# Performance work log

Hardware: AMD Instinct MI355X
Metric: run time of the kernel (lower is better)

The kernel has to match this reference:

```python
import jax, jax.numpy as jnp
import numpy as np

HIDDEN = 2048
N_HEADS = 32
N_KV = 8
HEAD_DIM = HIDDEN // N_HEADS  # 64
GROUP = N_HEADS // N_KV       # 4
FFN = 8192
EPS = 1e-5
ROPE_BASE = 500000.0
NEG = -1e9


def rms_norm(x, w, eps=EPS):
    var = jnp.mean(x * x, axis=-1, keepdims=True)
    return x * jax.lax.rsqrt(var + eps) * w


def rope_cos_sin(position_ids):
    # inv_freq: [head_dim//2]
    inv_freq = 1.0 / (ROPE_BASE ** (jnp.arange(0, HEAD_DIM, 2, dtype=jnp.float32) / HEAD_DIM))
    freqs = position_ids.astype(jnp.float32)[:, :, None] * inv_freq[None, None, :]  # [b,s,d/2]
    emb = jnp.concatenate([freqs, freqs], axis=-1)  # [b,s,d]
    return jnp.cos(emb), jnp.sin(emb)


def rotate_half(x):
    x1, x2 = jnp.split(x, 2, axis=-1)
    return jnp.concatenate([-x2, x1], axis=-1)


def setup_inputs() -> dict:
    key = jax.random.key(0)
    ks = jax.random.split(key, 12)
    b, s = 2, 1024
    scale_h = 1.0 / np.sqrt(HIDDEN)
    scale_f = 1.0 / np.sqrt(FFN)
    hidden_states = jax.random.normal(ks[0], (b, s, HIDDEN), jnp.float32)
    causal = jnp.where(jnp.tril(jnp.ones((s, s), bool)), 0.0, NEG).astype(jnp.float32)
    attention_mask = jnp.broadcast_to(causal[None, None], (b, 1, s, s))
    position_ids = jnp.broadcast_to(jnp.arange(s, dtype=jnp.int32)[None], (b, s))
    return {
        "hidden_states": hidden_states,
        "attention_mask": attention_mask,
        "wq": jax.random.normal(ks[1], (HIDDEN, N_HEADS * HEAD_DIM), jnp.float32) * scale_h,
        "wk": jax.random.normal(ks[2], (HIDDEN, N_KV * HEAD_DIM), jnp.float32) * scale_h,
        "wv": jax.random.normal(ks[3], (HIDDEN, N_KV * HEAD_DIM), jnp.float32) * scale_h,
        "wo": jax.random.normal(ks[4], (N_HEADS * HEAD_DIM, HIDDEN), jnp.float32) * scale_h,
        "norm1_w": jnp.ones((HIDDEN,), jnp.float32),
        "norm2_w": jnp.ones((HIDDEN,), jnp.float32),
        "w_gate": jax.random.normal(ks[5], (HIDDEN, FFN), jnp.float32) * scale_h,
        "w_up": jax.random.normal(ks[6], (HIDDEN, FFN), jnp.float32) * scale_h,
        "w_down": jax.random.normal(ks[7], (FFN, HIDDEN), jnp.float32) * scale_f,
        "position_ids": position_ids,
    }


def reference(hidden_states, attention_mask, wq, wk, wv, wo, norm1_w, norm2_w,
              w_gate, w_up, w_down, position_ids):
    b, s, _ = hidden_states.shape
    residual = hidden_states
    normed = rms_norm(hidden_states, norm1_w)

    q = (normed @ wq).reshape(b, s, N_HEADS, HEAD_DIM).transpose(0, 2, 1, 3)  # [b,H,s,d]
    k = (normed @ wk).reshape(b, s, N_KV, HEAD_DIM).transpose(0, 2, 1, 3)    # [b,G,s,d]
    v = (normed @ wv).reshape(b, s, N_KV, HEAD_DIM).transpose(0, 2, 1, 3)

    cos, sin = rope_cos_sin(position_ids)  # [b,s,d]
    cos, sin = cos[:, None], sin[:, None]  # unsqueeze head dim
    q = q * cos + rotate_half(q) * sin
    k = k * cos + rotate_half(k) * sin

    # repeat_kv: [b,G,s,d] -> [b,H,s,d]
    k = jnp.repeat(k, GROUP, axis=1)
    v = jnp.repeat(v, GROUP, axis=1)

    scores = jnp.einsum('bhqd,bhkd->bhqk', q, k)
    scores = scores + attention_mask  # mask added BEFORE scaling, as in source
    attn = jax.nn.softmax(scores / np.sqrt(HEAD_DIM), axis=-1)
    ctx = jnp.einsum('bhqk,bhkd->bhqd', attn, v)
    ctx = ctx.transpose(0, 2, 1, 3).reshape(b, s, N_HEADS * HEAD_DIM)
    attn_out = ctx @ wo

    normed_ff = rms_norm(attn_out + residual, norm2_w)
    ff = (jax.nn.silu(normed_ff @ w_gate) * (normed_ff @ w_up)) @ w_down
    return attn_out + ff
```

## Files before the change

### kernel.cpp

```cpp
#include <hip/hip_runtime.h>
#include <hip/hip_bf16.h>
#include <cstddef>
#include <cstdint>

#define T_TOK   2048
#define HID     2048
#define NHEADS  32
#define NKV     8
#define HDIM    64
#define FFN_DIM 8192
#define QKV_N   3072

typedef __hip_bfloat16 bf16;
typedef __attribute__((ext_vector_type(8))) short short8;
typedef __attribute__((ext_vector_type(4))) float f32x4;
typedef __attribute__((ext_vector_type(4))) unsigned short us4;

typedef __attribute__((address_space(1))) const void cg_void;
typedef __attribute__((address_space(3))) void lds_void;

__global__ __launch_bounds__(256) void cast_transpose(const float* __restrict__ in,
                                                      bf16* __restrict__ out,
                                                      int K, int N)
{
    __shared__ bf16 t[64][65];
    const int n0 = blockIdx.x * 64, k0 = blockIdx.y * 64;
    const int tn = threadIdx.x & 63, tk = threadIdx.x >> 6;
    #pragma unroll
    for (int kk = tk; kk < 64; kk += 4)
        t[kk][tn] = __float2bfloat16(in[(size_t)(k0 + kk) * N + n0 + tn]);
    __syncthreads();
    #pragma unroll
    for (int nn = tk; nn < 64; nn += 4)
        out[(size_t)(n0 + nn) * K + k0 + tn] = t[tn][nn];
}

__global__ __launch_bounds__(256) void cast_ilv(const float* __restrict__ in,
                                                bf16* __restrict__ out,
                                                int N, int is_up)
{
    __shared__ bf16 t[64][65];
    const int n0 = blockIdx.x * 64, k0 = blockIdx.y * 64;
    const int tn = threadIdx.x & 63, tk = threadIdx.x >> 6;
    #pragma unroll
    for (int kk = tk; kk < 64; kk += 4)
        t[kk][tn] = __float2bfloat16(in[(size_t)(k0 + kk) * N + n0 + tn]);
    __syncthreads();
    #pragma unroll
    for (int nn = tk; nn < 64; nn += 4) {
        int n = n0 + nn;
        int r = ((n >> 5) << 6) + (is_up << 5) + (n & 31);
        out[(size_t)r * HID + k0 + tn] = t[tn][nn];
    }
}

__global__ __launch_bounds__(256) void rmsnorm_kernel(const float* __restrict__ x,
                                                      const float* __restrict__ w,
                                                      bf16* __restrict__ out)
{
    __shared__ float sm[4];
    const int row = blockIdx.x, tid = threadIdx.x;
    const float4* xr = (const float4*)(x + (size_t)row * HID);
    float4 a = xr[tid], b = xr[tid + 256];
    float ss = a.x*a.x + a.y*a.y + a.z*a.z + a.w*a.w
             + b.x*b.x + b.y*b.y + b.z*b.z + b.w*b.w;
    #pragma unroll
    for (int off = 32; off; off >>= 1) ss += __shfl_down(ss, off);
    if ((tid & 63) == 0) sm[tid >> 6] = ss;
    __syncthreads();
    float sc = rsqrtf((sm[0] + sm[1] + sm[2] + sm[3]) * (1.0f / HID) + 1e-5f);
    const float4* wr = (const float4*)w;
    float4 w0 = wr[tid], w1 = wr[tid + 256];
    bf16* o = out + (size_t)row * HID;
    o[tid*4+0] = __float2bfloat16(a.x * sc * w0.x);
    o[tid*4+1] = __float2bfloat16(a.y * sc * w0.y);
    o[tid*4+2] = __float2bfloat16(a.z * sc * w0.z);
    o[tid*4+3] = __float2bfloat16(a.w * sc * w0.w);
    o[1024+tid*4+0] = __float2bfloat16(b.x * sc * w1.x);
    o[1024+tid*4+1] = __float2bfloat16(b.y * sc * w1.y);
    o[1024+tid*4+2] = __float2bfloat16(b.z * sc * w1.z);
    o[1024+tid*4+3] = __float2bfloat16(b.w * sc * w1.w);
}

__global__ __launch_bounds__(256) void rmsnorm_add_kernel(const float* __restrict__ xa,
                                                          const float* __restrict__ xb,
                                                          const float* __restrict__ w,
                                                          bf16* __restrict__ out)
{
    __shared__ float sm[4];
    const int row = blockIdx.x, tid = threadIdx.x;
    const float4* ar = (const float4*)(xa + (size_t)row * HID);
    const float4* br = (const float4*)(xb + (size_t)row * HID);
    float4 a0 = ar[tid], a1 = ar[tid + 256];
    float4 b0 = br[tid], b1 = br[tid + 256];
    float4 s0, s1;
    s0.x = a0.x + b0.x; s0.y = a0.y + b0.y; s0.z = a0.z + b0.z; s0.w = a0.w + b0.w;
    s1.x = a1.x + b1.x; s1.y = a1.y + b1.y; s1.z = a1.z + b1.z; s1.w = a1.w + b1.w;
    float ss = s0.x*s0.x + s0.y*s0.y + s0.z*s0.z + s0.w*s0.w
             + s1.x*s1.x + s1.y*s1.y + s1.z*s1.z + s1.w*s1.w;
    #pragma unroll
    for (int off = 32; off; off >>= 1) ss += __shfl_down(ss, off);
    if ((tid & 63) == 0) sm[tid >> 6] = ss;
    __syncthreads();
    float sc = rsqrtf((sm[0] + sm[1] + sm[2] + sm[3]) * (1.0f / HID) + 1e-5f);
    const float4* wr = (const float4*)w;
    float4 w0 = wr[tid], w1 = wr[tid + 256];
    bf16* o = out + (size_t)row * HID;
    o[tid*4+0] = __float2bfloat16(s0.x * sc * w0.x);
    o[tid*4+1] = __float2bfloat16(s0.y * sc * w0.y);
    o[tid*4+2] = __float2bfloat16(s0.z * sc * w0.z);
    o[tid*4+3] = __float2bfloat16(s0.w * sc * w0.w);
    o[1024+tid*4+0] = __float2bfloat16(s1.x * sc * w1.x);
    o[1024+tid*4+1] = __float2bfloat16(s1.y * sc * w1.y);
    o[1024+tid*4+2] = __float2bfloat16(s1.z * sc * w1.z);
    o[1024+tid*4+3] = __float2bfloat16(s1.w * sc * w1.w);
}

template<int BN, int EPI>
__device__ __forceinline__ void gemm_body(
    const bf16* __restrict__ A, const bf16* __restrict__ Bt,
    float* __restrict__ Cf,
    int lda, int kbeg, int klen, int ldc, int bx, int by)
{
    constexpr int NFR   = BN / 32;
    constexpr int CALLS = 4 + NFR;
    __shared__ bf16 As[2 * 128 * 64];
    __shared__ bf16 Bs[2 * BN * 64];
    const int tid = threadIdx.x;
    const int wv = tid >> 6, ln = tid & 63;
    const int wr = wv >> 1, wc = wv & 1;
    const size_t m0 = (size_t)by * 128;
    const size_t n0 = (size_t)bx * BN;

    const int lrow = ln >> 3;
    const int lk   = (ln & 7) ^ lrow;

    const bf16* Abase = A  + (m0 + (size_t)wv*32 + lrow) * lda + kbeg + lk*8;
    const bf16* Bbase = Bt + (n0 + (size_t)wv*NFR*8 + lrow) * lda + kbeg + lk*8;
    bf16* AsW = As + wv*2048;
    bf16* BsW = Bs + wv*NFR*512;

    auto stage = [&](int p, int tk) {
        #pragma unroll
        for (int i = 0; i < 4; ++i)
            __builtin_amdgcn_global_load_lds((cg_void*)(Abase + (size_t)i*8*lda + tk),
                                             (lds_void*)(AsW + p*8192 + i*512), 16, 0, 0);
        #pragma unroll
        for (int i = 0; i < NFR; ++i)
            __builtin_amdgcn_global_load_lds((cg_void*)(Bbase + (size_t)i*8*lda + tk),
                                             (lds_void*)(BsW + p*(BN*64) + i*512), 16, 0, 0);
    };

    f32x4 acc[4][NFR] = {};
    const int nt = klen >> 6;

    stage(0, 0);
    stage(1, 64);
    asm volatile("s_waitcnt vmcnt(%0)" :: "n"(CALLS) : "memory");
    __builtin_amdgcn_sched_barrier(0);
    __builtin_amdgcn_s_barrier();

    for (int t = 0; t < nt; ++t) {
        const int p = t & 1;
        const char* Ab = (const char*)As + p * 16384;
        const char* Bb = (const char*)Bs + p * (BN * 128);

        short8 af[4][2], bfr[NFR][2];
        #pragma unroll
        for (int ks = 0; ks < 2; ++ks) {
            const int kbyte = ks*64 + (ln >> 4)*16;
            #pragma unroll
            for (int m = 0; m < 4; ++m) {
                int row = wr*64 + m*16 + (ln & 15);
                af[m][ks] = *(const short8*)(Ab + row*128 + (kbyte ^ ((row & 7) << 4)));
            }
            #pragma unroll
            for (int n = 0; n < NFR; ++n) {
                int row = wc*(BN/2) + n*16 + (ln & 15);
                bfr[n][ks] = *(const short8*)(Bb + row*128 + (kbyte ^ ((row & 7) << 4)));
            }
        }
        asm volatile("s_waitcnt lgkmcnt(0)" ::: "memory");
        __builtin_amdgcn_sched_barrier(0);
        __builtin_amdgcn_s_barrier();

        const bool more = (t + 2 < nt);
        if (more) stage(p, (t + 2) * 64);
        __builtin_amdgcn_sched_barrier(0);

        __builtin_amdgcn_s_setprio(1);
        #pragma unroll
        for (int ks = 0; ks < 2; ++ks)
            #pragma unroll
            for (int m = 0; m < 4; ++m)
                #pragma unroll
                for (int n = 0; n < NFR; ++n)
                    acc[m][n] = __builtin_amdgcn_mfma_f32_16x16x32_bf16(af[m][ks], bfr[n][ks], acc[m][n], 0, 0, 0);
        __builtin_amdgcn_s_setprio(0);

        if (more) { asm volatile("s_waitcnt vmcnt(%0)" :: "n"(CALLS) : "memory"); }
        else      { asm volatile("s_waitcnt vmcnt(0)" ::: "memory"); }
        __builtin_amdgcn_sched_barrier(0);
        __builtin_amdgcn_s_barrier();
    }

    const int cj = ln & 15, rj = ln >> 4;
    #pragma unroll
    for (int m = 0; m < 4; ++m) {
        #pragma unroll
        for (int j = 0; j < 4; ++j) {
            size_t row = m0 + wr*64 + m*16 + rj*4 + j;
            #pragma unroll
            for (int n = 0; n < NFR; ++n) {
                int col = (int)n0 + wc*(BN/2) + n*16 + cj;
                float v = acc[m][n][j];
                size_t off = row * (size_t)ldc + col;
                if constexpr (EPI == 0) Cf[off] = v;
                else if constexpr (EPI == 5) unsafeAtomicAdd(&Cf[off], v);
            }
        }
    }
}

__device__ __forceinline__ void swz(int& bx, int& by) {
    const int nwg = gridDim.x * gridDim.y;
    int orig = blockIdx.y * gridDim.x + blockIdx.x;
    int wg = (orig & 7) * (nwg >> 3) + (orig >> 3);
    by = wg % gridDim.y;
    bx = wg / gridDim.y;
}

__global__ __launch_bounds__(256) void g_qkv(const bf16* __restrict__ A,
                                             const bf16* __restrict__ Bt,
                                             float* __restrict__ C) {
    int bx, by; swz(bx, by);
    gemm_body<64,0>(A, Bt, C, HID, 0, HID, QKV_N, bx, by);
}
__global__ __launch_bounds__(256) void g_wo(const bf16* __restrict__ A,
                                            const bf16* __restrict__ Bt,
                                            float* __restrict__ C) {
    int bx, by; swz(bx, by);
    gemm_body<64,0>(A, Bt, C, HID, 0, HID, HID, bx, by);
}
__global__ __launch_bounds__(256) void g_down(const bf16* __restrict__ A,
                                              const bf16* __restrict__ Bt,
                                              float* __restrict__ C) {
    int bx, by; swz(bx, by);
    gemm_body<64,5>(A, Bt, C, FFN_DIM, blockIdx.z * 4096, 4096, HID, bx, by);
}

__global__ __launch_bounds__(512, 2) void g_gateup(const bf16* __restrict__ A,
                                                   const bf16* __restrict__ Bt,
                                                   bf16* __restrict__ C)
{
    __shared__ bf16 As[2 * 256 * 64];
    __shared__ bf16 Bs[2 * 256 * 64];
    const int tid = threadIdx.x;
    const int wv = tid >> 6, ln = tid & 63;
    const int wr = wv >> 2, wc = wv & 3;

    const int nwg = gridDim.x * gridDim.y;
    int orig = blockIdx.y * gridDim.x + blockIdx.x;
    int wg = (orig & 7) * (nwg >> 3) + (orig >> 3);
    const int by = wg % gridDim.y, bx = wg / gridDim.y;
    const size_t m0 = (size_t)by * 256;
    const size_t n0 = (size_t)bx * 256;

    const int lrow = ln >> 3;
    const int lk   = (ln & 7) ^ lrow;

    const bf16* Abase = A  + (m0 + (size_t)wv*32 + lrow) * HID + lk*8;
    const bf16* Bbase = Bt + (n0 + (size_t)wv*32 + lrow) * HID + lk*8;
    bf16* AsW = As + wv*2048;
    bf16* BsW = Bs + wv*2048;

    auto stage = [&](int p, int tk) {
        #pragma unroll
        for (int i = 0; i < 4; ++i)
            __builtin_amdgcn_global_load_lds((cg_void*)(Abase + (size_t)i*8*HID + tk),
                                             (lds_void*)(AsW + p*16384 + i*512), 16, 0, 0);
        #pragma unroll
        for (int i = 0; i < 4; ++i)
            __builtin_amdgcn_global_load_lds((cg_void*)(Bbase + (size_t)i*8*HID + tk),
                                             (lds_void*)(BsW + p*16384 + i*512), 16, 0, 0);
    };

    f32x4 acc[8][4] = {};
    constexpr int nt = HID / 64;

    stage(0, 0);
    stage(1, 64);
    asm volatile("s_waitcnt vmcnt(8)" ::: "memory");
    __builtin_amdgcn_sched_barrier(0);
    __builtin_amdgcn_s_barrier();

    for (int t = 0; t < nt; ++t) {
        const int p = t & 1;
        const char* Ab = (const char*)As + p * 32768;
        const char* Bb = (const char*)Bs + p * 32768;

        short8 af[8], bf[4];
        {
            const int kbyte = (ln >> 4) * 16;
            #pragma unroll
            for (int m = 0; m < 8; ++m) {
                int row = wr*128 + m*16 + (ln & 15);
                af[m] = *(const short8*)(Ab + row*128 + (kbyte ^ ((row & 7) << 4)));
            }
            #pragma unroll
            for (int n = 0; n < 4; ++n) {
                int row = wc*64 + n*16 + (ln & 15);
                bf[n] = *(const short8*)(Bb + row*128 + (kbyte ^ ((row & 7) << 4)));
            }
        }
        asm volatile("s_waitcnt lgkmcnt(0)" ::: "memory");
        __builtin_amdgcn_sched_barrier(0);
        __builtin_amdgcn_s_setprio(1);
        #pragma unroll
        for (int m = 0; m < 8; ++m)
            #pragma unroll
            for (int n = 0; n < 4; ++n)
                acc[m][n] = __builtin_amdgcn_mfma_f32_16x16x32_bf16(af[m], bf[n], acc[m][n], 0, 0, 0);
        __builtin_amdgcn_s_setprio(0);
        {
            const int kbyte = 64 + (ln >> 4) * 16;
            #pragma unroll
            for (int m = 0; m < 8; ++m) {
                int row = wr*128 + m*16 + (ln & 15);
                af[m] = *(const short8*)(Ab + row*128 + (kbyte ^ ((row & 7) << 4)));
            }
            #pragma unroll
            for (int n = 0; n < 4; ++n) {
                int row = wc*64 + n*16 + (ln & 15);
                bf[n] = *(const short8*)(Bb + row*128 + (kbyte ^ ((row & 7) << 4)));
            }
        }
        asm volatile("s_waitcnt lgkmcnt(0)" ::: "memory");
        __builtin_amdgcn_sched_barrier(0);
        __builtin_amdgcn_s_barrier();

        const bool more = (t + 2 < nt);
        if (more) stage(p, (t + 2) * 64);
        __builtin_amdgcn_sched_barrier(0);

        __builtin_amdgcn_s_setprio(1);
        #pragma unroll
        for (int m = 0; m < 8; ++m)
            #pragma unroll
            for (int n = 0; n < 4; ++n)
                acc[m][n] = __builtin_amdgcn_mfma_f32_16x16x32_bf16(af[m], bf[n], acc[m][n], 0, 0, 0);
        __builtin_amdgcn_s_setprio(0);

        if (more) { asm volatile("s_waitcnt vmcnt(8)" ::: "memory"); }
        else      { asm volatile("s_waitcnt vmcnt(0)" ::: "memory"); }
        __builtin_amdgcn_sched_barrier(0);
        __builtin_amdgcn_s_barrier();
    }

    const int cj = ln & 15, rj = ln >> 4;
    const int slab = (int)(n0 >> 6) + wc;
    #pragma unroll
    for (int m = 0; m < 8; ++m) {
        #pragma unroll
        for (int j = 0; j < 4; ++j) {
            size_t row = m0 + wr*128 + m*16 + rj*4 + j;
            #pragma unroll
            for (int n = 0; n < 2; ++n) {
                int col = slab*32 + n*16 + cj;
                float g = acc[m][n][j];
                float u = acc[m][n+2][j];
                C[row * (size_t)FFN_DIM + col] =
                    __float2bfloat16(g / (1.0f + __expf(-g)) * u);
            }
        }
    }
}

__global__ __launch_bounds__(256) void rope_cast(const float* __restrict__ qkv,
                                                 const int* __restrict__ pos_ids,
                                                 bf16* __restrict__ Qp,
                                                 bf16* __restrict__ Kp)
{
    const int t = blockIdx.x, tid = threadIdx.x;
    const int b = t >> 10, s = t & 1023;
    const float pos = (float)pos_ids[t];
    const float* row = qkv + (size_t)t * QKV_N;

    {
        int idx = tid * 4;
        int hq = idx >> 5, j = idx & 31;
        float xa[4], xb[4];
        *(float4*)xa = *(const float4*)(row + hq*64 + j);
        *(float4*)xb = *(const float4*)(row + hq*64 + j + 32);
        us4 o1, o2;
        #pragma unroll
        for (int jj = 0; jj < 4; ++jj) {
            float inv = exp2f(-(float)(j + jj) * 0.5916115177913804f);
            float ang = pos * inv, c, sn;
            sincosf(ang, &sn, &c);
            o1[jj] = __bfloat16_as_ushort(__float2bfloat16(xa[jj]*c - xb[jj]*sn));
            o2[jj] = __bfloat16_as_ushort(__float2bfloat16(xb[jj]*c + xa[jj]*sn));
        }
        bf16* qd = Qp + ((size_t)(b*32 + hq)*1024 + s)*64;
        *(us4*)(qd + j)      = o1;
        *(us4*)(qd + j + 32) = o2;
    }
    {
        int hk = tid >> 5, j = tid & 31;
        float a = row[2048 + hk*64 + j];
        float bb = row[2048 + hk*64 + j + 32];
        float inv = exp2f(-(float)j * 0.5916115177913804f);
        float ang = pos * inv, c, sn;
        sincosf(ang, &sn, &c);
        bf16* kd = Kp + ((size_t)(b*8 + hk)*1024 + s)*64;
        kd[j]      = __float2bfloat16(a*c - bb*sn);
        kd[j + 32] = __float2bfloat16(bb*c + a*sn);
    }
}

__global__ __launch_bounds__(256) void vt_cast(const float* __restrict__ qkv,
                                               bf16* __restrict__ Vt)
{
    __shared__ bf16 tile[64][64];
    const int s0 = blockIdx.x * 64;
    const int sec = blockIdx.y;
    const int b = sec >> 3, hk = sec & 7;
    const int tid = threadIdx.x;
    const float* base = qkv + ((size_t)(b*1024 + s0)) * QKV_N + 2560 + hk*64;
    const int srow = tid >> 2, d0 = (tid & 3) * 16;
    #pragma unroll
    for (int q = 0; q < 4; ++q) {
        float va[4];
        *(float4*)va = *(const float4*)(base + (size_t)srow * QKV_N + d0 + q*4);
        #pragma unroll
        for (int cc = 0; cc < 4; ++cc)
            tile[d0 + q*4 + cc][srow] = __float2bfloat16(va[cc]);
    }
    __syncthreads();
    const int dr = tid >> 2, sc = (tid & 3) * 16;
    bf16* od = Vt + ((size_t)sec*64 + dr)*1024 + s0 + sc;
    *(short8*)od       = *(const short8*)&tile[dr][sc];
    *(short8*)(od + 8) = *(const short8*)&tile[dr][sc + 8];
}

__global__ __launch_bounds__(256) void attn_mfma(const bf16* __restrict__ Qp,
                                                 const bf16* __restrict__ Kp,
                                                 const bf16* __restrict__ Vt,
                                                 bf16* __restrict__ ctx)
{
    __shared__ bf16 Ks[128 * 64];
    __shared__ bf16 Vs[64 * 128];
    __shared__ bf16 Ps[4 * 32 * 128];
    const int tid = threadIdx.x;
    const int w = tid >> 6, ln = tid & 63;
    const int qt = blockIdx.x, h = blockIdx.y, b = blockIdx.z;
    const int hk = h >> 2;
    const int q0 = qt * 128;

    const bf16* qsec = Qp + ((size_t)(b*32 + h)*1024 + q0 + w*32)*64;
    const bf16* ksec = Kp + ((size_t)(b*8 + hk)*1024)*64;
    const bf16* vsec = Vt + ((size_t)(b*8 + hk))*64*1024;

    short8 qf[2][2];
    #pragma unroll
    for (int f = 0; f < 2; ++f)
        #pragma unroll
        for (int kc = 0; kc < 2; ++kc)
            qf[f][kc] = *(const short8*)(qsec + (size_t)(f*16 + (ln & 15))*64 + kc*32 + (ln >> 4)*8);

    f32x4 acc_o[2][4] = {};
    f32x4 m[2], l[2];
    #pragma unroll
    for (int f = 0; f < 2; ++f)
        #pragma unroll
        for (int j = 0; j < 4; ++j) { m[f][j] = -1e30f; l[f][j] = 0.0f; }

    const int lrow = ln >> 3;
    const int lkk  = (ln & 7) ^ lrow;
    char* PsW = (char*)Ps + w * 8192;

    const int ntiles = qt + 1;
    for (int kt = 0; kt < ntiles; ++kt) {
        const int kv0 = kt * 128;
        {
            const bf16* kbase = ksec + (size_t)(kv0 + w*32 + lrow)*64 + lkk*8;
            bf16* KsW = Ks + w*2048;
            #pragma unroll
            for (int i = 0; i < 4; ++i)
                __builtin_amdgcn_global_load_lds((cg_void*)(kbase + (size_t)i*8*64),
                                                 (lds_void*)(KsW + i*512), 16, 0, 0);
        }
        {
            bf16* VsW = Vs + w*2048;
            #pragma unroll
            for (int i = 0; i < 4; ++i) {
                int d = w*16 + i*4 + (ln >> 4);
                __builtin_amdgcn_global_load_lds(
                    (cg_void*)(vsec + (size_t)d*1024 + kv0 + (((ln & 15) ^ (d & 7))*8)),
                    (lds_void*)(VsW + i*512), 16, 0, 0);
            }
        }
        __syncthreads();

        f32x4 acc_s[2][8] = {};
        #pragma unroll
        for (int c = 0; c < 8; ++c) {
            int kvr = c*16 + (ln & 15);
            const char* krow = (const char*)Ks + kvr*128;
            short8 kf0 = *(const short8*)(krow + (((ln >> 4)*16)      ^ ((kvr & 7) << 4)));
            short8 kf1 = *(const short8*)(krow + ((64 + (ln >> 4)*16) ^ ((kvr & 7) << 4)));
            #pragma unroll
            for (int f = 0; f < 2; ++f) {
                acc_s[f][c] = __builtin_amdgcn_mfma_f32_16x16x32_bf16(qf[f][0], kf0, acc_s[f][c], 0, 0, 0);
                acc_s[f][c] = __builtin_amdgcn_mfma_f32_16x16x32_bf16(qf[f][1], kf1, acc_s[f][c], 0, 0, 0);
            }
        }

        const bool diag = (kt == qt);
        f32x4 vmax[2];
        #pragma unroll
        for (int f = 0; f < 2; ++f)
            #pragma unroll
            for (int j = 0; j < 4; ++j) vmax[f][j] = -1e30f;
        #pragma unroll
        for (int f = 0; f < 2; ++f) {
            #pragma unroll
            for (int c = 0; c < 8; ++c) {
                f32x4 t = acc_s[f][c] * 0.125f;
                if (diag) {
                    int kv = kv0 + c*16 + (ln & 15);
                    int qg = q0 + w*32 + f*16 + (ln >> 4)*4;
                    #pragma unroll
                    for (int j = 0; j < 4; ++j)
                        if (kv > qg + j) t[j] = -1e30f;
                }
                acc_s[f][c] = t;
                #pragma unroll
                for (int j = 0; j < 4; ++j) vmax[f][j] = fmaxf(vmax[f][j], t[j]);
            }
            #pragma unroll
            for (int mk = 1; mk <= 8; mk <<= 1)
                #pragma unroll
                for (int j = 0; j < 4; ++j)
                    vmax[f][j] = fmaxf(vmax[f][j], __shfl_xor(vmax[f][j], mk));
        }

        #pragma unroll
        for (int f = 0; f < 2; ++f) {
            f32x4 r;
            #pragma unroll
            for (int j = 0; j < 4; ++j) {
                float mn = fmaxf(m[f][j], vmax[f][j]);
                r[j] = __expf(m[f][j] - mn);
                m[f][j] = mn;
                l[f][j] *= r[j];
            }
            #pragma unroll
            for (int df = 0; df < 4; ++df)
                #pragma unroll
                for (int j = 0; j < 4; ++j) acc_o[f][df][j] *= r[j];
        }

        f32x4 rs[2] = {};
        #pragma unroll
        for (int f = 0; f < 2; ++f) {
            #pragma unroll
            for (int c = 0; c < 8; ++c) {
                #pragma unroll
                for (int j = 0; j < 4; ++j) {
                    float p = __expf(acc_s[f][c][j] - m[f][j]);
                    rs[f][j] += p;
                    int qloc = f*16 + (ln >> 4)*4 + j;
                    int kvb  = (c*16 + (ln & 15))*2;
                    *(bf16*)(PsW + qloc*256 + (kvb ^ ((qloc & 7) << 4))) = __float2bfloat16(p);
                }
            }
            #pragma unroll
            for (int mk = 1; mk <= 8; mk <<= 1)
                #pragma unroll
                for (int j = 0; j < 4; ++j)
                    rs[f][j] += __shfl_xor(rs[f][j], mk);
            #pragma unroll
            for (int j = 0; j < 4; ++j) l[f][j] += rs[f][j];
        }

        #pragma unroll
        for (int kc = 0; kc < 4; ++kc) {
            short8 pa[2];
            #pragma unroll
            for (int f = 0; f < 2; ++f) {
                int qloc = f*16 + (ln & 15);
                pa[f] = *(const short8*)(PsW + qloc*256 + ((kc*64 + (ln >> 4)*16) ^ ((qloc & 7) << 4)));
            }
            #pragma unroll
            for (int df = 0; df < 4; ++df) {
                int dl = df*16 + (ln & 15);
                short8 vfr = *(const short8*)((const char*)Vs + dl*256 + ((kc*64 + (ln >> 4)*16) ^ ((dl & 7) << 4)));
                #pragma unroll
                for (int f = 0; f < 2; ++f)
                    acc_o[f][df] = __builtin_amdgcn_mfma_f32_16x16x32_bf16(pa[f], vfr, acc_o[f][df], 0, 0, 0);
            }
        }
        __syncthreads();
    }

    #pragma unroll
    for (int f = 0; f < 2; ++f) {
        f32x4 inv;
        #pragma unroll
        for (int j = 0; j < 4; ++j) inv[j] = 1.0f / l[f][j];
        #pragma unroll
        for (int df = 0; df < 4; ++df) {
            #pragma unroll
            for (int j = 0; j < 4; ++j) {
                int q = q0 + w*32 + f*16 + (ln >> 4)*4 + j;
                int d = df*16 + (ln & 15);
                ctx[((size_t)b*1024 + q)*HID + h*64 + d] = __float2bfloat16(acc_o[f][df][j] * inv[j]);
            }
        }
    }
}

extern "C" void kernel_launch(void* const* d_in, const int* in_sizes, int n_in,
                              void* d_out, int out_size, void* d_ws, size_t ws_size,
                              hipStream_t stream)
{
    const float* hidden = (const float*)d_in[0];
    const float* wq = (const float*)d_in[2];
    const float* wk = (const float*)d_in[3];
    const float* wv = (const float*)d_in[4];
    const float* wo = (const float*)d_in[5];
    const float* n1 = (const float*)d_in[6];
    const float* n2 = (const float*)d_in[7];
    const float* wg = (const float*)d_in[8];
    const float* wu = (const float*)d_in[9];
    const float* wd = (const float*)d_in[10];
    const int*  pos = (const int*)d_in[11];
    float* out = (float*)d_out;
    char* ws = (char*)d_ws;

    bf16* wgu_t  = (bf16*)(ws + 0);
    bf16* wd_t   = (bf16*)(ws + 67108864);
    bf16* wqkv_t = (bf16*)(ws + 100663296);
    bf16* wo_t   = (bf16*)(ws + 113246208);
    bf16* normed = (bf16*)(ws + 121634816);
    float* qkv   = (float*)(ws + 130023424);
    bf16* ctx    = (bf16*)(ws + 155189248);
    bf16* hb     = (bf16*)(ws + 130023424);
    bf16* Qp     = (bf16*)(ws + 121634816);
    bf16* Kp     = (bf16*)(ws + 163577856);
    bf16* Vt     = (bf16*)(ws + 165675008);

    cast_transpose<<<dim3(32, 32), 256, 0, stream>>>(wq, wqkv_t, 2048, 2048);
    cast_transpose<<<dim3(8, 32),  256, 0, stream>>>(wk, wqkv_t + 4194304, 2048, 512);
    cast_transpose<<<dim3(8, 32),  256, 0, stream>>>(wv, wqkv_t + 5242880, 2048, 512);
    cast_transpose<<<dim3(32, 32), 256, 0, stream>>>(wo, wo_t, 2048, 2048);
    cast_ilv<<<dim3(128, 32), 256, 0, stream>>>(wg, wgu_t, FFN_DIM, 0);
    cast_ilv<<<dim3(128, 32), 256, 0, stream>>>(wu, wgu_t, FFN_DIM, 1);
    cast_transpose<<<dim3(32, 128),256, 0, stream>>>(wd, wd_t, 8192, 2048);

    rmsnorm_kernel<<<T_TOK, 256, 0, stream>>>(hidden, n1, normed);
    g_qkv<<<dim3(QKV_N/64, T_TOK/128), 256, 0, stream>>>(normed, wqkv_t, qkv);
    rope_cast<<<T_TOK, 256, 0, stream>>>(qkv, pos, Qp, Kp);
    vt_cast<<<dim3(16, 16), 256, 0, stream>>>(qkv, Vt);
    attn_mfma<<<dim3(8, NHEADS, 2), 256, 0, stream>>>(Qp, Kp, Vt, ctx);
    g_wo<<<dim3(HID/64, T_TOK/128), 256, 0, stream>>>(ctx, wo_t, out);
    rmsnorm_add_kernel<<<T_TOK, 256, 0, stream>>>(out, hidden, n2, normed);
    g_gateup<<<dim3(16384/256, T_TOK/256), 512, 0, stream>>>(normed, wgu_t, hb);
    g_down<<<dim3(HID/64, T_TOK/128, 2), 256, 0, stream>>>(hb, wd_t, out);
}
```

Measured before the change: 515.1 us.

## Generalize 256x256 GEMM with finer-grained load interleaving and reuse it for down-projection

Turns the 256x256-tile gate/up GEMM into a templated body. The body splits each K-tile into four quadrant sub-steps and issues the next tile's global-to-LDS loads in pieces between them, instead of one bulk stage per tile, so memory traffic overlaps more evenly with MFMA work. The down-projection now uses this 512-thread, 256-tile body with a 4-way split-K and atomic-add epilogue, replacing the 128x64-tile kernel with 2-way split-K. Extra barriers per quadrant and more atomic traffic on the output are the added costs.

```diff
diff --git a/kernel.cpp b/kernel.cpp
--- a/kernel.cpp
+++ b/kernel.cpp
@@ -213,10 +213,7 @@
             #pragma unroll
             for (int n = 0; n < NFR; ++n) {
                 int col = (int)n0 + wc*(BN/2) + n*16 + cj;
-                float v = acc[m][n][j];
-                size_t off = row * (size_t)ldc + col;
-                if constexpr (EPI == 0) Cf[off] = v;
-                else if constexpr (EPI == 5) unsafeAtomicAdd(&Cf[off], v);
+                Cf[row * (size_t)ldc + col] = acc[m][n][j];
             }
         }
     }
@@ -242,138 +239,153 @@
     int bx, by; swz(bx, by);
     gemm_body<64,0>(A, Bt, C, HID, 0, HID, HID, bx, by);
 }
-__global__ __launch_bounds__(256) void g_down(const bf16* __restrict__ A,
-                                              const bf16* __restrict__ Bt,
-                                              float* __restrict__ C) {
-    int bx, by; swz(bx, by);
-    gemm_body<64,5>(A, Bt, C, FFN_DIM, blockIdx.z * 4096, 4096, HID, bx, by);
-}
-
-__global__ __launch_bounds__(512, 2) void g_gateup(const bf16* __restrict__ A,
-                                                   const bf16* __restrict__ Bt,
-                                                   bf16* __restrict__ C)
+
+template<int EPI>
+__device__ __forceinline__ void gemm256_body(
+    const bf16* __restrict__ A, const bf16* __restrict__ Bt,
+    float* __restrict__ Cf, bf16* __restrict__ Cb,
+    int lda, int kbeg, int klen, int ldc, int bx, int by)
 {
     __shared__ bf16 As[2 * 256 * 64];
     __shared__ bf16 Bs[2 * 256 * 64];
     const int tid = threadIdx.x;
     const int wv = tid >> 6, ln = tid & 63;
     const int wr = wv >> 2, wc = wv & 3;
-
+    const size_t m0 = (size_t)by * 256;
+    const size_t n0 = (size_t)bx * 256;
+
+    const int lrow = ln >> 3;
+    const int lk   = (ln & 7) ^ lrow;
+
+    auto stA = [&](int p, int tk, int i) {
+        const int r = ((i & 1) << 7) | ((i >> 1) << 6);
+        __builtin_amdgcn_global_load_lds(
+            (cg_void*)(A + (m0 + r + wv*8 + lrow) * lda + kbeg + tk + lk*8),
+            (lds_void*)(As + p*16384 + (r + wv*8) * 64), 16, 0, 0);
+    };
+    auto stB = [&](int p, int tk, int j) {
+        const int r = ((wv >> 1) << 6) + ((wv & 1) << 3) + ((j & 1) << 4) + ((j >> 1) << 5);
+        __builtin_amdgcn_global_load_lds(
+            (cg_void*)(Bt + (n0 + r + lrow) * lda + kbeg + tk + lk*8),
+            (lds_void*)(Bs + p*16384 + r * 64), 16, 0, 0);
+    };
+
+    f32x4 acc[8][4] = {};
+    const int nt = klen >> 6;
+
+    #pragma unroll
+    for (int i = 0; i < 4; ++i) { stA(0, 0, i); stB(0, 0, i); }
+    stA(1, 64, 0); stA(1, 64, 1); stB(1, 64, 0); stB(1, 64, 1);
+    asm volatile("s_waitcnt vmcnt(4)" ::: "memory");
+    __builtin_amdgcn_sched_barrier(0);
+    __builtin_amdgcn_s_barrier();
+
+    for (int t = 0; t < nt; ++t) {
+        const int p = t & 1;
+        const char* Ab = (const char*)As + p * 32768;
+        const char* Bb = (const char*)Bs + p * 32768;
+        const int tk1 = (t + 1) * 64, tk2 = (t + 2) * 64;
+        const bool m1 = (t + 1 < nt), m2 = (t + 2 < nt);
+
+        #pragma unroll
+        for (int q = 0; q < 4; ++q) {
+            const int mh = q >> 1, nh = q & 1;
+            short8 af[4][2], bfr[2][2];
+            #pragma unroll
+            for (int ks = 0; ks < 2; ++ks) {
+                const int kbyte = ks*64 + (ln >> 4)*16;
+                #pragma unroll
+                for (int m = 0; m < 4; ++m) {
+                    int row = wr*128 + (mh*4 + m)*16 + (ln & 15);
+                    af[m][ks] = *(const short8*)(Ab + row*128 + (kbyte ^ ((row & 7) << 4)));
+                }
+                #pragma unroll
+                for (int n = 0; n < 2; ++n) {
+                    int row = wc*64 + (nh*2 + n)*16 + (ln & 15);
+                    bfr[n][ks] = *(const short8*)(Bb + row*128 + (kbyte ^ ((row & 7) << 4)));
+                }
+            }
+            if (q == 0 && m1) { stA(p ^ 1, tk1, 2); stA(p ^ 1, tk1, 3); }
+            if (q == 1 && m1) { stB(p ^ 1, tk1, 2); stB(p ^ 1, tk1, 3); }
+            if (q == 2 && m2) { stA(p, tk2, 0); stA(p, tk2, 1); }
+            if (q == 3 && m2) { stB(p, tk2, 0); stB(p, tk2, 1); }
+            __builtin_amdgcn_sched_barrier(0);
+            __builtin_amdgcn_s_barrier();
+            asm volatile("s_waitcnt lgkmcnt(0)" ::: "memory");
+            __builtin_amdgcn_sched_barrier(0);
+            __builtin_amdgcn_s_setprio(1);
+            #pragma unroll
+            for (int ks = 0; ks < 2; ++ks)
+                #pragma unroll
+                for (int m = 0; m < 4; ++m)
+                    #pragma unroll
+                    for (int n = 0; n < 2; ++n)
+                        acc[mh*4 + m][nh*2 + n] = __builtin_amdgcn_mfma_f32_16x16x32_bf16(
+                            af[m][ks], bfr[n][ks], acc[mh*4 + m][nh*2 + n], 0, 0, 0);
+            __builtin_amdgcn_s_setprio(0);
+            __builtin_amdgcn_sched_barrier(0);
+            __builtin_amdgcn_s_barrier();
+        }
+        if (m2) { asm volatile("s_waitcnt vmcnt(4)" ::: "memory"); }
+        else    { asm volatile("s_waitcnt vmcnt(0)" ::: "memory"); }
+        __builtin_amdgcn_sched_barrier(0);
+        __builtin_amdgcn_s_barrier();
+    }
+
+    const int cj = ln & 15, rj = ln >> 4;
+    if constexpr (EPI == 4) {
+        const int slab = (int)(n0 >> 6) + wc;
+        #pragma unroll
+        for (int m = 0; m < 8; ++m) {
+            #pragma unroll
+            for (int j = 0; j < 4; ++j) {
+                size_t row = m0 + wr*128 + m*16 + rj*4 + j;
+                #pragma unroll
+                for (int n = 0; n < 2; ++n) {
+                    int col = slab*32 + n*16 + cj;
+                    float g = acc[m][n][j];
+                    float u = acc[m][n+2][j];
+                    Cb[row * (size_t)ldc + col] =
+                        __float2bfloat16(g / (1.0f + __expf(-g)) * u);
+                }
+            }
+        }
+    } else {
+        #pragma unroll
+        for (int m = 0; m < 8; ++m) {
+            #pragma unroll
+            for (int j = 0; j < 4; ++j) {
+                size_t row = m0 + wr*128 + m*16 + rj*4 + j;
+                #pragma unroll
+                for (int n = 0; n < 4; ++n) {
+                    int col = (int)n0 + wc*64 + n*16 + cj;
+                    unsafeAtomicAdd(&Cf[row * (size_t)ldc + col], acc[m][n][j]);
+                }
+            }
+        }
+    }
+}
+
+__global__ __launch_bounds__(512, 2) void g_gateup(const bf16* __restrict__ A,
+                                                   const bf16* __restrict__ Bt,
+                                                   bf16* __restrict__ C)
+{
     const int nwg = gridDim.x * gridDim.y;
     int orig = blockIdx.y * gridDim.x + blockIdx.x;
     int wg = (orig & 7) * (nwg >> 3) + (orig >> 3);
     const int by = wg % gridDim.y, bx = wg / gridDim.y;
-    const size_t m0 = (size_t)by * 256;
-    const size_t n0 = (size_t)bx * 256;
-
-    const int lrow = ln >> 3;
-    const int lk   = (ln & 7) ^ lrow;
-
-    const bf16* Abase = A  + (m0 + (size_t)wv*32 + lrow) * HID + lk*8;
-    const bf16* Bbase = Bt + (n0 + (size_t)wv*32 + lrow) * HID + lk*8;
-    bf16* AsW = As + wv*2048;
-    bf16* BsW = Bs + wv*2048;
-
-    auto stage = [&](int p, int tk) {
-        #pragma unroll
-        for (int i = 0; i < 4; ++i)
-            __builtin_amdgcn_global_load_lds((cg_void*)(Abase + (size_t)i*8*HID + tk),
-                                             (lds_void*)(AsW + p*16384 + i*512), 16, 0, 0);
-        #pragma unroll
-        for (int i = 0; i < 4; ++i)
-            __builtin_amdgcn_global_load_lds((cg_void*)(Bbase + (size_t)i*8*HID + tk),
-                                             (lds_void*)(BsW + p*16384 + i*512), 16, 0, 0);
-    };
-
-    f32x4 acc[8][4] = {};
-    constexpr int nt = HID / 64;
-
-    stage(0, 0);
-    stage(1, 64);
-    asm volatile("s_waitcnt vmcnt(8)" ::: "memory");
-    __builtin_amdgcn_sched_barrier(0);
-    __builtin_amdgcn_s_barrier();
-
-    for (int t = 0; t < nt; ++t) {
-        const int p = t & 1;
-        const char* Ab = (const char*)As + p * 32768;
-        const char* Bb = (const char*)Bs + p * 32768;
-
-        short8 af[8], bf[4];
-        {
-            const int kbyte = (ln >> 4) * 16;
-            #pragma unroll
-            for (int m = 0; m < 8; ++m) {
-                int row = wr*128 + m*16 + (ln & 15);
-                af[m] = *(const short8*)(Ab + row*128 + (kbyte ^ ((row & 7) << 4)));
-            }
-            #pragma unroll
-            for (int n = 0; n < 4; ++n) {
-                int row = wc*64 + n*16 + (ln & 15);
-                bf[n] = *(const short8*)(Bb + row*128 + (kbyte ^ ((row & 7) << 4)));
-            }
-        }
-        asm volatile("s_waitcnt lgkmcnt(0)" ::: "memory");
-        __builtin_amdgcn_sched_barrier(0);
-        __builtin_amdgcn_s_setprio(1);
-        #pragma unroll
-        for (int m = 0; m < 8; ++m)
-            #pragma unroll
-            for (int n = 0; n < 4; ++n)
-                acc[m][n] = __builtin_amdgcn_mfma_f32_16x16x32_bf16(af[m], bf[n], acc[m][n], 0, 0, 0);
-        __builtin_amdgcn_s_setprio(0);
-        {
-            const int kbyte = 64 + (ln >> 4) * 16;
-            #pragma unroll
-            for (int m = 0; m < 8; ++m) {
-                int row = wr*128 + m*16 + (ln & 15);
-                af[m] = *(const short8*)(Ab + row*128 + (kbyte ^ ((row & 7) << 4)));
-            }
-            #pragma unroll
-            for (int n = 0; n < 4; ++n) {
-                int row = wc*64 + n*16 + (ln & 15);
-                bf[n] = *(const short8*)(Bb + row*128 + (kbyte ^ ((row & 7) << 4)));
-            }
-        }
-        asm volatile("s_waitcnt lgkmcnt(0)" ::: "memory");
-        __builtin_amdgcn_sched_barrier(0);
-        __builtin_amdgcn_s_barrier();
-
-        const bool more = (t + 2 < nt);
-        if (more) stage(p, (t + 2) * 64);
-        __builtin_amdgcn_sched_barrier(0);
-
-        __builtin_amdgcn_s_setprio(1);
-        #pragma unroll
-        for (int m = 0; m < 8; ++m)
-            #pragma unroll
-            for (int n = 0; n < 4; ++n)
-                acc[m][n] = __builtin_amdgcn_mfma_f32_16x16x32_bf16(af[m], bf[n], acc[m][n], 0, 0, 0);
-        __builtin_amdgcn_s_setprio(0);
-
-        if (more) { asm volatile("s_waitcnt vmcnt(8)" ::: "memory"); }
-        else      { asm volatile("s_waitcnt vmcnt(0)" ::: "memory"); }
-        __builtin_amdgcn_sched_barrier(0);
-        __builtin_amdgcn_s_barrier();
-    }
-
-    const int cj = ln & 15, rj = ln >> 4;
-    const int slab = (int)(n0 >> 6) + wc;
-    #pragma unroll
-    for (int m = 0; m < 8; ++m) {
-        #pragma unroll
-        for (int j = 0; j < 4; ++j) {
-            size_t row = m0 + wr*128 + m*16 + rj*4 + j;
-            #pragma unroll
-            for (int n = 0; n < 2; ++n) {
-                int col = slab*32 + n*16 + cj;
-                float g = acc[m][n][j];
-                float u = acc[m][n+2][j];
-                C[row * (size_t)FFN_DIM + col] =
-                    __float2bfloat16(g / (1.0f + __expf(-g)) * u);
-            }
-        }
-    }
+    gemm256_body<4>(A, Bt, nullptr, C, HID, 0, HID, FFN_DIM, bx, by);
+}
+
+__global__ __launch_bounds__(512, 2) void g_down(const bf16* __restrict__ A,
+                                                 const bf16* __restrict__ Bt,
+                                                 float* __restrict__ C)
+{
+    const int nwg = gridDim.x * gridDim.y;
+    int orig = blockIdx.y * gridDim.x + blockIdx.x;
+    int wg = (orig & 7) * (nwg >> 3) + (orig >> 3);
+    const int by = wg % gridDim.y, bx = wg / gridDim.y;
+    gemm256_body<5>(A, Bt, C, nullptr, FFN_DIM, blockIdx.z * 2048, 2048, HID, bx, by);
 }
 
 __global__ __launch_bounds__(256) void rope_cast(const float* __restrict__ qkv,
@@ -667,5 +679,5 @@
     g_wo<<<dim3(HID/64, T_TOK/128), 256, 0, stream>>>(ctx, wo_t, out);
     rmsnorm_add_kernel<<<T_TOK, 256, 0, stream>>>(out, hidden, n2, normed);
     g_gateup<<<dim3(16384/256, T_TOK/256), 512, 0, stream>>>(normed, wgu_t, hb);
-    g_down<<<dim3(HID/64, T_TOK/128, 2), 256, 0, stream>>>(hb, wd_t, out);
-}
+    g_down<<<dim3(HID/256, T_TOK/256, 4), 512, 0, stream>>>(hb, wd_t, out);
+}
```

Result: slower. 568.4 us (+10.3%).

## Run down-projection on 256x256 tile GEMM body with split-K of four

Applied to the files above, without the earlier changes.

Generalizes the gate/up 256x256 GEMM kernel into a templated body with runtime lda, K offset and length, and an atomic-add epilogue. The down projection uses it with split-K 4 instead of the 128x64 tile kernel with split-K 2. The goal is better operand reuse per block and higher MFMA density for the largest GEMM. In exchange the output sees more atomic partial sums, and the grid is smaller, with fewer k-iterations per block.

```diff
diff --git a/kernel.cpp b/kernel.cpp
--- a/kernel.cpp
+++ b/kernel.cpp
@@ -116,7 +116,7 @@
     o[1024+tid*4+3] = __float2bfloat16(s1.w * sc * w1.w);
 }
 
-template<int BN, int EPI>
+template<int BN>
 __device__ __forceinline__ void gemm_body(
     const bf16* __restrict__ A, const bf16* __restrict__ Bt,
     float* __restrict__ Cf,
@@ -213,10 +213,7 @@
             #pragma unroll
             for (int n = 0; n < NFR; ++n) {
                 int col = (int)n0 + wc*(BN/2) + n*16 + cj;
-                float v = acc[m][n][j];
-                size_t off = row * (size_t)ldc + col;
-                if constexpr (EPI == 0) Cf[off] = v;
-                else if constexpr (EPI == 5) unsafeAtomicAdd(&Cf[off], v);
+                Cf[row * (size_t)ldc + col] = acc[m][n][j];
             }
         }
     }
@@ -234,59 +231,50 @@
                                              const bf16* __restrict__ Bt,
                                              float* __restrict__ C) {
     int bx, by; swz(bx, by);
-    gemm_body<64,0>(A, Bt, C, HID, 0, HID, QKV_N, bx, by);
+    gemm_body<64>(A, Bt, C, HID, 0, HID, QKV_N, bx, by);
 }
 __global__ __launch_bounds__(256) void g_wo(const bf16* __restrict__ A,
                                             const bf16* __restrict__ Bt,
                                             float* __restrict__ C) {
     int bx, by; swz(bx, by);
-    gemm_body<64,0>(A, Bt, C, HID, 0, HID, HID, bx, by);
-}
-__global__ __launch_bounds__(256) void g_down(const bf16* __restrict__ A,
-                                              const bf16* __restrict__ Bt,
-                                              float* __restrict__ C) {
-    int bx, by; swz(bx, by);
-    gemm_body<64,5>(A, Bt, C, FFN_DIM, blockIdx.z * 4096, 4096, HID, bx, by);
-}
-
-__global__ __launch_bounds__(512, 2) void g_gateup(const bf16* __restrict__ A,
-                                                   const bf16* __restrict__ Bt,
-                                                   bf16* __restrict__ C)
+    gemm_body<64>(A, Bt, C, HID, 0, HID, HID, bx, by);
+}
+
+template<int EPI>
+__device__ __forceinline__ void gemm256_body(
+    const bf16* __restrict__ A, const bf16* __restrict__ Bt,
+    float* __restrict__ Cf, bf16* __restrict__ Cb,
+    int lda, int kbeg, int klen, int ldc, int bx, int by)
 {
     __shared__ bf16 As[2 * 256 * 64];
     __shared__ bf16 Bs[2 * 256 * 64];
     const int tid = threadIdx.x;
     const int wv = tid >> 6, ln = tid & 63;
     const int wr = wv >> 2, wc = wv & 3;
-
-    const int nwg = gridDim.x * gridDim.y;
-    int orig = blockIdx.y * gridDim.x + blockIdx.x;
-    int wg = (orig & 7) * (nwg >> 3) + (orig >> 3);
-    const int by = wg % gridDim.y, bx = wg / gridDim.y;
     const size_t m0 = (size_t)by * 256;
     const size_t n0 = (size_t)bx * 256;
 
     const int lrow = ln >> 3;
     const int lk   = (ln & 7) ^ lrow;
 
-    const bf16* Abase = A  + (m0 + (size_t)wv*32 + lrow) * HID + lk*8;
-    const bf16* Bbase = Bt + (n0 + (size_t)wv*32 + lrow) * HID + lk*8;
+    const bf16* Abase = A  + (m0 + (size_t)wv*32 + lrow) * lda + kbeg + lk*8;
+    const bf16* Bbase = Bt + (n0 + (size_t)wv*32 + lrow) * lda + kbeg + lk*8;
     bf16* AsW = As + wv*2048;
     bf16* BsW = Bs + wv*2048;
 
     auto stage = [&](int p, int tk) {
         #pragma unroll
         for (int i = 0; i < 4; ++i)
-            __builtin_amdgcn_global_load_lds((cg_void*)(Abase + (size_t)i*8*HID + tk),
+            __builtin_amdgcn_global_load_lds((cg_void*)(Abase + (size_t)i*8*lda + tk),
                                              (lds_void*)(AsW + p*16384 + i*512), 16, 0, 0);
         #pragma unroll
         for (int i = 0; i < 4; ++i)
-            __builtin_amdgcn_global_load_lds((cg_void*)(Bbase + (size_t)i*8*HID + tk),
+            __builtin_amdgcn_global_load_lds((cg_void*)(Bbase + (size_t)i*8*lda + tk),
                                              (lds_void*)(BsW + p*16384 + i*512), 16, 0, 0);
     };
 
     f32x4 acc[8][4] = {};
-    constexpr int nt = HID / 64;
+    const int nt = klen >> 6;
 
     stage(0, 0);
     stage(1, 64);
@@ -358,22 +346,59 @@
     }
 
     const int cj = ln & 15, rj = ln >> 4;
-    const int slab = (int)(n0 >> 6) + wc;
-    #pragma unroll
-    for (int m = 0; m < 8; ++m) {
-        #pragma unroll
-        for (int j = 0; j < 4; ++j) {
-            size_t row = m0 + wr*128 + m*16 + rj*4 + j;
-            #pragma unroll
-            for (int n = 0; n < 2; ++n) {
-                int col = slab*32 + n*16 + cj;
-                float g = acc[m][n][j];
-                float u = acc[m][n+2][j];
-                C[row * (size_t)FFN_DIM + col] =
-                    __float2bfloat16(g / (1.0f + __expf(-g)) * u);
-            }
-        }
-    }
+    if constexpr (EPI == 4) {
+        const int slab = (int)(n0 >> 6) + wc;
+        #pragma unroll
+        for (int m = 0; m < 8; ++m) {
+            #pragma unroll
+            for (int j = 0; j < 4; ++j) {
+                size_t row = m0 + wr*128 + m*16 + rj*4 + j;
+                #pragma unroll
+                for (int n = 0; n < 2; ++n) {
+                    int col = slab*32 + n*16 + cj;
+                    float g = acc[m][n][j];
+                    float u = acc[m][n+2][j];
+                    Cb[row * (size_t)ldc + col] =
+                        __float2bfloat16(g / (1.0f + __expf(-g)) * u);
+                }
+            }
+        }
+    } else {
+        #pragma unroll
+        for (int m = 0; m < 8; ++m) {
+            #pragma unroll
+            for (int j = 0; j < 4; ++j) {
+                size_t row = m0 + wr*128 + m*16 + rj*4 + j;
+                #pragma unroll
+                for (int n = 0; n < 4; ++n) {
+                    int col = (int)n0 + wc*64 + n*16 + cj;
+                    unsafeAtomicAdd(&Cf[row * (size_t)ldc + col], acc[m][n][j]);
+                }
+            }
+        }
+    }
+}
+
+__global__ __launch_bounds__(512, 2) void g_gateup(const bf16* __restrict__ A,
+                                                   const bf16* __restrict__ Bt,
+                                                   bf16* __restrict__ C)
+{
+    const int nwg = gridDim.x * gridDim.y;
+    int orig = blockIdx.y * gridDim.x + blockIdx.x;
+    int wg = (orig & 7) * (nwg >> 3) + (orig >> 3);
+    const int by = wg % gridDim.y, bx = wg / gridDim.y;
+    gemm256_body<4>(A, Bt, nullptr, C, HID, 0, HID, FFN_DIM, bx, by);
+}
+
+__global__ __launch_bounds__(512, 2) void g_down(const bf16* __restrict__ A,
+                                                 const bf16* __restrict__ Bt,
+                                                 float* __restrict__ C)
+{
+    const int nwg = gridDim.x * gridDim.y;
+    int orig = blockIdx.y * gridDim.x + blockIdx.x;
+    int wg = (orig & 7) * (nwg >> 3) + (orig >> 3);
+    const int by = wg % gridDim.y, bx = wg / gridDim.y;
+    gemm256_body<5>(A, Bt, C, nullptr, FFN_DIM, blockIdx.z * 2048, 2048, HID, bx, by);
 }
 
 __global__ __launch_bounds__(256) void rope_cast(const float* __restrict__ qkv,
@@ -667,5 +692,5 @@
     g_wo<<<dim3(HID/64, T_TOK/128), 256, 0, stream>>>(ctx, wo_t, out);
     rmsnorm_add_kernel<<<T_TOK, 256, 0, stream>>>(out, hidden, n2, normed);
     g_gateup<<<dim3(16384/256, T_TOK/256), 512, 0, stream>>>(normed, wgu_t, hb);
-    g_down<<<dim3(HID/64, T_TOK/128, 2), 256, 0, stream>>>(hb, wd_t, out);
-}
+    g_down<<<dim3(HID/256, T_TOK/256, 4), 512, 0, stream>>>(hb, wd_t, out);
+}
```

New measurement: 513.4 us. No clear change (-0.3%).
